# Kernel tuning notes

Hardware: AMD Instinct MI355X
Metric: run time of the kernel (lower is better)

Reference implementation:

```python
import jax, jax.numpy as jnp
import numpy as np

N = 100000   # nodes
E = 1600000  # edges (avg degree 16)
D = 256      # in_channels == dim (forward hard-codes BatchNorm1d(256))
BN_EPS = 1e-5


def _batchnorm(x, gamma, beta):
    # training-mode BatchNorm1d: batch statistics over node dim, biased variance
    mu = jnp.mean(x, axis=0)
    var = jnp.var(x, axis=0)
    return (x - mu) * jax.lax.rsqrt(var + BN_EPS) * gamma + beta


def _gin_conv(x, src, dst, n, W1, b1, gamma, beta, W2, b2):
    # GINConv, eps=0: nn((1+eps)*x + sum_{j in N(i)} x_j)
    agg = jax.ops.segment_sum(x[src], dst, num_segments=n)  # sparse neighbor sum
    h = x + agg
    h = jax.nn.relu(_batchnorm(h @ W1 + b1, gamma, beta))
    return jax.nn.relu(h @ W2 + b2)


def setup_inputs() -> dict:
    key = jax.random.key(0)
    ks = jax.random.split(key, 8)
    x = jax.random.normal(ks[0], (N, D), dtype=jnp.float32)
    edge_index = jax.random.randint(ks[1], (2, E), 0, N, dtype=jnp.int64)
    s = 0.02
    inp = {
        "x": x,
        "edge_index": edge_index,
        # fresh BatchNorm1d(256) in forward (default affine params)
        "g0": jnp.ones((D,), jnp.float32),
        "b0": jnp.zeros((D,), jnp.float32),
        # conv1 MLP: Linear-BN-ReLU-Linear-ReLU
        "W1a": jax.random.normal(ks[2], (D, D), jnp.float32) * s,
        "b1a": jnp.zeros((D,), jnp.float32),
        "g1": jnp.ones((D,), jnp.float32),
        "bt1": jnp.zeros((D,), jnp.float32),
        "W1b": jax.random.normal(ks[3], (D, D), jnp.float32) * s,
        "b1b": jnp.zeros((D,), jnp.float32),
        # conv2 MLP
        "W2a": jax.random.normal(ks[4], (D, D), jnp.float32) * s,
        "b2a": jnp.zeros((D,), jnp.float32),
        "g2": jnp.ones((D,), jnp.float32),
        "bt2": jnp.zeros((D,), jnp.float32),
        "W2b": jax.random.normal(ks[5], (D, D), jnp.float32) * s,
        "b2b": jnp.zeros((D,), jnp.float32),
    }
    return inp


def reference(x, edge_index, g0, b0, W1a, b1a, g1, bt1, W1b, b1b,
              W2a, b2a, g2, bt2, W2b, b2b):
    n = x.shape[0]
    src, dst = edge_index[0], edge_index[1]
    h = _batchnorm(x, g0, b0)                       # fresh BN(256) on input
    h = _gin_conv(h, src, dst, n, W1a, b1a, g1, bt1, W1b, b1b)
    h = jax.nn.relu(h)                              # outer relu (dropout=eval, identity)
    h = _gin_conv(h, src, dst, n, W2a, b2a, g2, bt2, W2b, b2b)
    return jax.nn.relu(h)
```

## Files before the change

### kernel.cpp

```cpp
#include <hip/hip_runtime.h>

#define N_NODES 100000
#define N_EDGES 1600000
#define DIM 256
#define NBINS 196
#define BINCAP 16384

typedef unsigned short bf16u;
typedef __attribute__((ext_vector_type(8))) short bf16x8s;
typedef __attribute__((ext_vector_type(4))) float f32x4;

__device__ __forceinline__ float bf2f(unsigned int u16) {
    union { unsigned int i; float f; } x; x.i = u16 << 16; return x.f;
}
__device__ __forceinline__ float hi2f(unsigned int u) {
    union { unsigned int i; float f; } x; x.i = u & 0xffff0000u; return x.f;
}
__device__ __forceinline__ float lo2f(unsigned int u) {
    union { unsigned int i; float f; } x; x.i = u << 16; return x.f;
}
__device__ __forceinline__ bf16u f2bf(float f) {
    union { float f; unsigned int i; } x; x.f = f;
    unsigned int i = x.i;
    return (bf16u)((i + 0x7fffu + ((i >> 16) & 1u)) >> 16);
}
__device__ __forceinline__ float loadv(const void* p, size_t i, int isf32) {
    return isf32 ? ((const float*)p)[i] : bf2f(((const bf16u*)p)[i]);
}
__device__ __forceinline__ void async_copy16(const void* g, void* l) {
    __builtin_amdgcn_global_load_lds((const __attribute__((address_space(1))) void*)g,
                                     (__attribute__((address_space(3))) void*)l, 16, 0, 0);
}

__global__ void detect_flags(const unsigned* xw, const int* ei, int* flags, int* gBinFill,
                             float* sums) {
    __shared__ int cnt, nz;
    if (threadIdx.x == 0) { cnt = 0; nz = 0; }
    __syncthreads();
    gBinFill[threadIdx.x] = 0;
#pragma unroll
    for (int i = 0; i < 6; ++i) sums[i * 256 + threadIdx.x] = 0.f;
    unsigned u = xw[threadIdx.x];
    float av = fabsf(bf2f(u & 0xffffu));
    if (av > 1e-5f && av < 50.f) atomicAdd(&cnt, 1);
    if (ei[2 * threadIdx.x + 1] != 0) atomicAdd(&nz, 1);
    __syncthreads();
    if (threadIdx.x == 0) {
        flags[0] = (cnt >= 128) ? 0 : 1;
        if (nz == 0) { flags[1] = 2; flags[2] = 2 * N_EDGES; }
        else         { flags[1] = 1; flags[2] = N_EDGES; }
    }
}

__global__ void transpose_w(const void* W0, const void* W1, const void* W2, const void* W3,
                            bf16u* Wt, const int* flags) {
    __shared__ bf16u tile[64][65];
    int isf32 = flags[0];
    const void* W = (blockIdx.y == 0) ? W0 : (blockIdx.y == 1) ? W1 : (blockIdx.y == 2) ? W2 : W3;
    bf16u* out = Wt + (size_t)blockIdx.y * DIM * DIM;
    int t = threadIdx.x;
    int tx = t & 63, ty = t >> 6;
    int k0 = (blockIdx.x >> 2) * 64, n0 = (blockIdx.x & 3) * 64;
#pragma unroll
    for (int i = 0; i < 16; ++i) {
        int r = ty + i * 4;
        tile[tx][r] = f2bf(loadv(W, (size_t)(k0 + r) * DIM + (n0 + tx), isf32));
    }
    __syncthreads();
#pragma unroll
    for (int i = 0; i < 16; ++i) {
        int r = ty + i * 4;
        out[(size_t)(n0 + r) * DIM + (k0 + tx)] = tile[r][tx];
    }
}

__global__ __launch_bounds__(256) void bin_scatter(const int* __restrict__ ei,
                                                   const int* __restrict__ flags,
                                                   uint2* __restrict__ gRec,
                                                   int* __restrict__ gBinFill) {
    __shared__ int cnt[256];
    __shared__ int cur[256];
    __shared__ uint2 rec[4096];
    int t = threadIdx.x;
    cnt[t] = 0; cur[t] = 0;
    __syncthreads();
    int st = flags[1], ofs = flags[2];
    int e0 = blockIdx.x * 4096;
#pragma unroll
    for (int i = 0; i < 16; ++i) {
        int e = e0 + i * 256 + t;
        uint2 r;
        if (e < N_EDGES) {
            r.x = (unsigned)ei[(size_t)ofs + (size_t)e * st];
            r.y = (unsigned)ei[(size_t)e * st];
            atomicAdd(&cnt[r.x >> 9], 1);
        } else {
            r.x = 0xffffffffu; r.y = 0;
        }
        rec[i * 256 + t] = r;
    }
    __syncthreads();
    if (t < NBINS) {
        int c = cnt[t];
        int b = (c > 0) ? atomicAdd(&gBinFill[t], c) : 0;
        cnt[t] = b;
    }
    __syncthreads();
#pragma unroll
    for (int i = 0; i < 16; ++i) {
        uint2 r = rec[i * 256 + t];
        if (r.x != 0xffffffffu) {
            int b = r.x >> 9;
            int li = atomicAdd(&cur[b], 1);
            int pos = cnt[b] + li;
            if (pos < BINCAP) gRec[(size_t)b * BINCAP + pos] = r;
        }
    }
}

__global__ void bin_scan(const int* gBinFill, int* binBase) {
    __shared__ int s[256];
    int t = threadIdx.x;
    s[t] = (t < NBINS) ? gBinFill[t] : 0;
    __syncthreads();
    for (int off = 1; off < 256; off <<= 1) {
        int v = (t >= off) ? s[t - off] : 0;
        __syncthreads();
        s[t] += v;
        __syncthreads();
    }
    binBase[t + 1] = s[t];
    if (t == 0) binBase[0] = 0;
}

__global__ __launch_bounds__(256) void bin_csr(const uint2* __restrict__ gRec,
                                               const int* __restrict__ gBinFill,
                                               const int* __restrict__ binBase,
                                               int* __restrict__ rp, int* __restrict__ col) {
    __shared__ int cntA[512], scanB[512], noff[512], ncur[512];
    int bin = blockIdx.x, t = threadIdx.x;
    int cnt = gBinFill[bin];
    if (cnt > BINCAP) cnt = BINCAP;
    int gbase = binBase[bin], lo = bin << 9;
    cntA[t] = 0; cntA[t + 256] = 0; ncur[t] = 0; ncur[t + 256] = 0;
    __syncthreads();
    const uint2* R = gRec + (size_t)bin * BINCAP;
    for (int j = t; j < cnt; j += 256) atomicAdd(&cntA[(int)R[j].x - lo], 1);
    __syncthreads();
    scanB[t] = cntA[t]; scanB[t + 256] = cntA[t + 256];
    __syncthreads();
    for (int off = 1; off < 512; off <<= 1) {
        int v0 = (t >= off) ? scanB[t - off] : 0;
        int v1 = (t + 256 >= off) ? scanB[t + 256 - off] : 0;
        __syncthreads();
        scanB[t] += v0; scanB[t + 256] += v1;
        __syncthreads();
    }
    noff[t] = scanB[t] - cntA[t];
    noff[t + 256] = scanB[t + 256] - cntA[t + 256];
    __syncthreads();
    int n0 = lo + t, n1 = lo + t + 256;
    if (n0 < N_NODES) rp[n0] = gbase + noff[t];
    if (n1 < N_NODES) rp[n1] = gbase + noff[t + 256];
    if (bin == 0 && t == 0) rp[N_NODES] = N_EDGES;
    for (int j = t; j < cnt; j += 256) {
        uint2 r = R[j];
        int k = (int)r.x - lo;
        int li = atomicAdd(&ncur[k], 1);
        col[gbase + noff[k] + li] = (int)r.y;
    }
}

__global__ void col_stats(const void* X, int nrows, float* sums, const int* flags, int dual) {
    __shared__ float ls[512];
    int isf32 = dual ? flags[0] : 0;
    int t = threadIdx.x;
    ls[t] = 0.f; ls[t + 256] = 0.f;
    __syncthreads();
    int rpb = (nrows + gridDim.x - 1) / gridDim.x;
    int r0 = blockIdx.x * rpb;
    int r1 = r0 + rpb; if (r1 > nrows) r1 = nrows;
    int cg = (t & 31) * 8;
    float s[8], q[8];
#pragma unroll
    for (int j = 0; j < 8; ++j) { s[j] = 0.f; q[j] = 0.f; }
    if (isf32) {
        for (int r = r0 + (t >> 5); r < r1; r += 8) {
            const float* xp = (const float*)X + (size_t)r * DIM + cg;
            f32x4 a = *(const f32x4*)xp, b = *(const f32x4*)(xp + 4);
#pragma unroll
            for (int j = 0; j < 4; ++j) {
                s[j] += a[j]; q[j] += a[j] * a[j];
                s[4 + j] += b[j]; q[4 + j] += b[j] * b[j];
            }
        }
    } else {
        for (int r = r0 + (t >> 5); r < r1; r += 8) {
            size_t base = (size_t)r * DIM + cg;
#pragma unroll
            for (int j = 0; j < 8; ++j) {
                float f = bf2f(((const bf16u*)X)[base + j]);
                s[j] += f; q[j] += f * f;
            }
        }
    }
#pragma unroll
    for (int j = 0; j < 8; ++j) {
        atomicAdd(&ls[cg + j], s[j]);
        atomicAdd(&ls[256 + cg + j], q[j]);
    }
    __syncthreads();
    atomicAdd(&sums[t], ls[t]);
    atomicAdd(&sums[256 + t], ls[256 + t]);
}

__global__ void bn_finalize(const float* sums, const void* gamma, const void* beta,
                            float* sc, float* sh, float inv_n, const int* flags) {
    int isf32 = flags[0];
    int t = threadIdx.x;
    float mu = sums[t] * inv_n;
    float var = sums[256 + t] * inv_n - mu * mu;
    float rs = rsqrtf(var + 1e-5f);
    float g = loadv(gamma, t, isf32), b = loadv(beta, t, isf32);
    sc[t] = rs * g;
    sh[t] = b - mu * rs * g;
}

__global__ void bn_apply(const void* X, const float* sc, const float* sh, bf16u* Y,
                         const int* flags, int dual, int relu) {
    int isf32 = dual ? flags[0] : 0;
    size_t i = (size_t)blockIdx.x * 256 + threadIdx.x;
    int c = ((int)(i & 31)) * 8;
    size_t base = i * 8;
    float v[8];
    if (isf32) {
        f32x4 x0 = *(const f32x4*)((const float*)X + base);
        f32x4 x1 = *(const f32x4*)((const float*)X + base + 4);
#pragma unroll
        for (int j = 0; j < 4; ++j) { v[j] = x0[j]; v[4 + j] = x1[j]; }
    } else {
        uint4 u = *(const uint4*)((const bf16u*)X + base);
        v[0] = lo2f(u.x); v[1] = hi2f(u.x);
        v[2] = lo2f(u.y); v[3] = hi2f(u.y);
        v[4] = lo2f(u.z); v[5] = hi2f(u.z);
        v[6] = lo2f(u.w); v[7] = hi2f(u.w);
    }
    f32x4 s0 = *(const f32x4*)(sc + c), s1 = *(const f32x4*)(sc + c + 4);
    f32x4 h0 = *(const f32x4*)(sh + c), h1 = *(const f32x4*)(sh + c + 4);
    float y[8];
#pragma unroll
    for (int j = 0; j < 4; ++j) {
        y[j]     = v[j]     * s0[j] + h0[j];
        y[4 + j] = v[4 + j] * s1[j] + h1[j];
    }
    if (relu) {
#pragma unroll
        for (int j = 0; j < 8; ++j) y[j] = fmaxf(y[j], 0.f);
    }
    uint4 ov;
    ov.x = (unsigned)f2bf(y[0]) | ((unsigned)f2bf(y[1]) << 16);
    ov.y = (unsigned)f2bf(y[2]) | ((unsigned)f2bf(y[3]) << 16);
    ov.z = (unsigned)f2bf(y[4]) | ((unsigned)f2bf(y[5]) << 16);
    ov.w = (unsigned)f2bf(y[6]) | ((unsigned)f2bf(y[7]) << 16);
    *(uint4*)(Y + base) = ov;
}

__global__ __launch_bounds__(512) void agg_gemm(const bf16u* __restrict__ h,
                                                const int* __restrict__ rp,
                                                const int* __restrict__ col,
                                                const bf16u* __restrict__ Wt,
                                                const void* __restrict__ bias,
                                                bf16u* __restrict__ Cout,
                                                const int* __restrict__ flags,
                                                float* __restrict__ stats) {
    __shared__ __align__(16) bf16u aggA[64 * 256];
    __shared__ __align__(16) bf16u Bs[4 * 256 * 8];
    __shared__ float lsum[512];
    int isf32 = flags[0];
    int t = threadIdx.x;
    int w = t >> 6, lane = t & 63;
    lsum[t] = 0.f;
    int rb = blockIdx.x * 64;

#pragma unroll
    for (int j = 0; j < 2; ++j) {
        int idx = w * 2 + j;
        int chunk = idx & 3, r0 = (idx >> 2) * 64;
        async_copy16(Wt + (size_t)(r0 + lane) * 256 + chunk * 8,
                     &Bs[chunk * 2048 + r0 * 8]);
    }

    {
        int p = lane >> 5, c = lane & 31;
        const uint4* hv = (const uint4*)h;
        for (int i = 0; i < 8; ++i) {
            int lrow = w * 8 + i;
            int node = rb + lrow;
            if (node >= N_NODES) node = N_NODES - 1;
            float acc[8];
            if (p == 0) {
                uint4 u = hv[(size_t)node * 32 + c];
                acc[0] = lo2f(u.x); acc[1] = hi2f(u.x);
                acc[2] = lo2f(u.y); acc[3] = hi2f(u.y);
                acc[4] = lo2f(u.z); acc[5] = hi2f(u.z);
                acc[6] = lo2f(u.w); acc[7] = hi2f(u.w);
            } else {
#pragma unroll
                for (int j = 0; j < 8; ++j) acc[j] = 0.f;
            }
            int e = rp[node], e1 = rp[node + 1];
            for (; e + 8 <= e1; e += 8) {
                int s0 = col[e + p], s1 = col[e + 2 + p], s2 = col[e + 4 + p], s3 = col[e + 6 + p];
                uint4 a = hv[(size_t)s0 * 32 + c];
                uint4 b = hv[(size_t)s1 * 32 + c];
                uint4 d = hv[(size_t)s2 * 32 + c];
                uint4 f = hv[(size_t)s3 * 32 + c];
                acc[0] += lo2f(a.x); acc[1] += hi2f(a.x); acc[2] += lo2f(a.y); acc[3] += hi2f(a.y);
                acc[4] += lo2f(a.z); acc[5] += hi2f(a.z); acc[6] += lo2f(a.w); acc[7] += hi2f(a.w);
                acc[0] += lo2f(b.x); acc[1] += hi2f(b.x); acc[2] += lo2f(b.y); acc[3] += hi2f(b.y);
                acc[4] += lo2f(b.z); acc[5] += hi2f(b.z); acc[6] += lo2f(b.w); acc[7] += hi2f(b.w);
                acc[0] += lo2f(d.x); acc[1] += hi2f(d.x); acc[2] += lo2f(d.y); acc[3] += hi2f(d.y);
                acc[4] += lo2f(d.z); acc[5] += hi2f(d.z); acc[6] += lo2f(d.w); acc[7] += hi2f(d.w);
                acc[0] += lo2f(f.x); acc[1] += hi2f(f.x); acc[2] += lo2f(f.y); acc[3] += hi2f(f.y);
                acc[4] += lo2f(f.z); acc[5] += hi2f(f.z); acc[6] += lo2f(f.w); acc[7] += hi2f(f.w);
            }
            for (; e + 4 <= e1; e += 4) {
                int s0 = col[e + p], s1 = col[e + 2 + p];
                uint4 a = hv[(size_t)s0 * 32 + c];
                uint4 b = hv[(size_t)s1 * 32 + c];
                acc[0] += lo2f(a.x); acc[1] += hi2f(a.x); acc[2] += lo2f(a.y); acc[3] += hi2f(a.y);
                acc[4] += lo2f(a.z); acc[5] += hi2f(a.z); acc[6] += lo2f(a.w); acc[7] += hi2f(a.w);
                acc[0] += lo2f(b.x); acc[1] += hi2f(b.x); acc[2] += lo2f(b.y); acc[3] += hi2f(b.y);
                acc[4] += lo2f(b.z); acc[5] += hi2f(b.z); acc[6] += lo2f(b.w); acc[7] += hi2f(b.w);
            }
            for (; e < e1; e += 2) {
                int idx = e + p;
                if (idx < e1) {
                    uint4 a = hv[(size_t)col[idx] * 32 + c];
                    acc[0] += lo2f(a.x); acc[1] += hi2f(a.x); acc[2] += lo2f(a.y); acc[3] += hi2f(a.y);
                    acc[4] += lo2f(a.z); acc[5] += hi2f(a.z); acc[6] += lo2f(a.w); acc[7] += hi2f(a.w);
                }
            }
#pragma unroll
            for (int j = 0; j < 8; ++j) acc[j] += __shfl_xor(acc[j], 32);
            if (p == 0) {
                uint4 ov;
                ov.x = (unsigned)f2bf(acc[0]) | ((unsigned)f2bf(acc[1]) << 16);
                ov.y = (unsigned)f2bf(acc[2]) | ((unsigned)f2bf(acc[3]) << 16);
                ov.z = (unsigned)f2bf(acc[4]) | ((unsigned)f2bf(acc[5]) << 16);
                ov.w = (unsigned)f2bf(acc[6]) | ((unsigned)f2bf(acc[7]) << 16);
                *(uint4*)&aggA[lrow * 256 + ((c ^ (lrow & 7)) * 8)] = ov;
            }
        }
    }

    int lr = lane & 15, lq = lane >> 4;
    int wm = w >> 2, wn = w & 3;
    f32x4 acc[2][4] = {};
    for (int kk = 0; kk < 8; ++kk) {
        __syncthreads();
        if (kk > 0) {
#pragma unroll
            for (int j = 0; j < 2; ++j) {
                int idx = w * 2 + j;
                int chunk = idx & 3, r0 = (idx >> 2) * 64;
                async_copy16(Wt + (size_t)(r0 + lane) * 256 + kk * 32 + chunk * 8,
                             &Bs[chunk * 2048 + r0 * 8]);
            }
        }
        __syncthreads();
        bf16x8s af[2], bfv[4];
#pragma unroll
        for (int mt = 0; mt < 2; ++mt) {
            int ar = wm * 32 + mt * 16 + lr;
            int kc = kk * 4 + lq;
            af[mt] = *(const bf16x8s*)&aggA[ar * 256 + ((kc ^ (lr & 7)) * 8)];
        }
#pragma unroll
        for (int nt = 0; nt < 4; ++nt) {
            int br = wn * 64 + nt * 16 + lr;
            bfv[nt] = *(const bf16x8s*)&Bs[lq * 2048 + br * 8];
        }
#pragma unroll
        for (int mt = 0; mt < 2; ++mt)
#pragma unroll
            for (int nt = 0; nt < 4; ++nt)
                acc[mt][nt] = __builtin_amdgcn_mfma_f32_16x16x32_bf16(af[mt], bfv[nt], acc[mt][nt], 0, 0, 0);
    }

#pragma unroll
    for (int nt = 0; nt < 4; ++nt) {
        int c = wn * 64 + nt * 16 + lr;
        float bv = loadv(bias, c, isf32);
        float ssum = 0.f, ssq = 0.f;
#pragma unroll
        for (int mt = 0; mt < 2; ++mt) {
            int r0 = rb + wm * 32 + mt * 16 + lq * 4;
#pragma unroll
            for (int j = 0; j < 4; ++j) {
                int r = r0 + j;
                if (r < N_NODES) {
                    float y = acc[mt][nt][j] + bv;
                    Cout[(size_t)r * 256 + c] = f2bf(y);
                    ssum += y; ssq += y * y;
                }
            }
        }
        atomicAdd(&lsum[c], ssum);
        atomicAdd(&lsum[256 + c], ssq);
    }
    __syncthreads();
    if (t < 256) {
        atomicAdd(&stats[t], lsum[t]);
        atomicAdd(&stats[256 + t], lsum[256 + t]);
    }
}

__global__ __launch_bounds__(256) void gemm_bias(const bf16u* __restrict__ A,
                                                 const bf16u* __restrict__ Wt,
                                                 const void* __restrict__ bias,
                                                 void* __restrict__ Cout, int mrows,
                                                 const int* __restrict__ flags,
                                                 int relu, int f32out,
                                                 float* __restrict__ stats,
                                                 const float* __restrict__ bnsc,
                                                 const float* __restrict__ bnsh) {
    __shared__ bf16u As[2][128 * 64];
    __shared__ bf16u Bs[2][128 * 64];
    __shared__ float lsum[256];
    int isf32 = flags[0];
    int t = threadIdx.x;
    int w = t >> 6, lane = t & 63;
    int lr = lane & 15, lq = lane >> 4;
    int wm = w >> 1, wn = w & 1;
    int xcd = blockIdx.x & 7, j0 = blockIdx.x >> 3;
    int wkid = ((xcd < 4) ? xcd * 196 : 784 + (xcd - 4) * 195) + j0;
    int rowBase = (wkid >> 1) * 128, colBase = (wkid & 1) * 128;
    f32x4 acc[4][4] = {};
    lsum[t] = 0.f;
    int srow = t >> 3;
    int g8   = ((t & 7) ^ ((t >> 3) & 7)) * 8;
    int ldsOff = (t >> 3) * 64 + (t & 7) * 8;

    if (bnsc) {
        f32x4 s0v = *(const f32x4*)(bnsc + g8);
        f32x4 s1v = *(const f32x4*)(bnsc + g8 + 4);
        f32x4 h0v = *(const f32x4*)(bnsh + g8);
        f32x4 h1v = *(const f32x4*)(bnsh + g8 + 4);
#pragma unroll
        for (int p = 0; p < 4; ++p) {
            int r = p * 32 + srow;
            int gr = rowBase + r; gr = (gr < mrows) ? gr : (mrows - 1);
            uint4 av = *(const uint4*)(A + (size_t)gr * 256 + g8);
            uint4 ov;
            ov.x = (unsigned)f2bf(fmaxf(lo2f(av.x) * s0v[0] + h0v[0], 0.f)) |
                   ((unsigned)f2bf(fmaxf(hi2f(av.x) * s0v[1] + h0v[1], 0.f)) << 16);
            ov.y = (unsigned)f2bf(fmaxf(lo2f(av.y) * s0v[2] + h0v[2], 0.f)) |
                   ((unsigned)f2bf(fmaxf(hi2f(av.y) * s0v[3] + h0v[3], 0.f)) << 16);
            ov.z = (unsigned)f2bf(fmaxf(lo2f(av.z) * s1v[0] + h1v[0], 0.f)) |
                   ((unsigned)f2bf(fmaxf(hi2f(av.z) * s1v[1] + h1v[1], 0.f)) << 16);
            ov.w = (unsigned)f2bf(fmaxf(lo2f(av.w) * s1v[2] + h1v[2], 0.f)) |
                   ((unsigned)f2bf(fmaxf(hi2f(av.w) * s1v[3] + h1v[3], 0.f)) << 16);
            *(uint4*)&As[0][p * 2048 + ldsOff] = ov;
            async_copy16(Wt + (size_t)(colBase + r) * 256 + g8, &Bs[0][(p * 32 + (w << 3)) * 64]);
        }
    } else {
#pragma unroll
        for (int p = 0; p < 4; ++p) {
            int r = p * 32 + srow;
            int gr = rowBase + r; gr = (gr < mrows) ? gr : (mrows - 1);
            async_copy16(A + (size_t)gr * 256 + g8, &As[0][(p * 32 + (w << 3)) * 64]);
            async_copy16(Wt + (size_t)(colBase + r) * 256 + g8, &Bs[0][(p * 32 + (w << 3)) * 64]);
        }
    }

    for (int kt = 0; kt < 4; ++kt) {
        int b = kt & 1, bn = b ^ 1;
        int kn = (kt + 1) * 64;
        __syncthreads();
        uint4 av[4];
        if (kt < 3) {
            if (bnsc) {
#pragma unroll
                for (int p = 0; p < 4; ++p) {
                    int r = p * 32 + srow;
                    int gr = rowBase + r; gr = (gr < mrows) ? gr : (mrows - 1);
                    av[p] = *(const uint4*)(A + (size_t)gr * 256 + kn + g8);
                }
#pragma unroll
                for (int p = 0; p < 4; ++p) {
                    int r = p * 32 + srow;
                    async_copy16(Wt + (size_t)(colBase + r) * 256 + kn + g8,
                                 &Bs[bn][(p * 32 + (w << 3)) * 64]);
                }
            } else {
#pragma unroll
                for (int p = 0; p < 4; ++p) {
                    int r = p * 32 + srow;
                    int gr = rowBase + r; gr = (gr < mrows) ? gr : (mrows - 1);
                    async_copy16(A + (size_t)gr * 256 + kn + g8,
                                 &As[bn][(p * 32 + (w << 3)) * 64]);
                    async_copy16(Wt + (size_t)(colBase + r) * 256 + kn + g8,
                                 &Bs[bn][(p * 32 + (w << 3)) * 64]);
                }
            }
        }
#pragma unroll
        for (int ks = 0; ks < 2; ++ks) {
            bf16x8s af[4], bfv[4];
#pragma unroll
            for (int mt = 0; mt < 4; ++mt) {
                int ar = wm * 64 + mt * 16 + lr;
                af[mt] = *(const bf16x8s*)&As[b][ar * 64 + (((ks * 4 + lq) ^ (lr & 7)) * 8)];
            }
#pragma unroll
            for (int nt = 0; nt < 4; ++nt) {
                int br = wn * 64 + nt * 16 + lr;
                bfv[nt] = *(const bf16x8s*)&Bs[b][br * 64 + (((ks * 4 + lq) ^ (lr & 7)) * 8)];
            }
#pragma unroll
            for (int mt = 0; mt < 4; ++mt)
#pragma unroll
                for (int nt = 0; nt < 4; ++nt)
                    acc[mt][nt] = __builtin_amdgcn_mfma_f32_16x16x32_bf16(af[mt], bfv[nt], acc[mt][nt], 0, 0, 0);
        }
        if (bnsc && kt < 3) {
            f32x4 s0v = *(const f32x4*)(bnsc + kn + g8);
            f32x4 s1v = *(const f32x4*)(bnsc + kn + g8 + 4);
            f32x4 h0v = *(const f32x4*)(bnsh + kn + g8);
            f32x4 h1v = *(const f32x4*)(bnsh + kn + g8 + 4);
#pragma unroll
            for (int p = 0; p < 4; ++p) {
                uint4 ov;
                ov.x = (unsigned)f2bf(fmaxf(lo2f(av[p].x) * s0v[0] + h0v[0], 0.f)) |
                       ((unsigned)f2bf(fmaxf(hi2f(av[p].x) * s0v[1] + h0v[1], 0.f)) << 16);
                ov.y = (unsigned)f2bf(fmaxf(lo2f(av[p].y) * s0v[2] + h0v[2], 0.f)) |
                       ((unsigned)f2bf(fmaxf(hi2f(av[p].y) * s0v[3] + h0v[3], 0.f)) << 16);
                ov.z = (unsigned)f2bf(fmaxf(lo2f(av[p].z) * s1v[0] + h1v[0], 0.f)) |
                       ((unsigned)f2bf(fmaxf(hi2f(av[p].z) * s1v[1] + h1v[1], 0.f)) << 16);
                ov.w = (unsigned)f2bf(fmaxf(lo2f(av[p].w) * s1v[2] + h1v[2], 0.f)) |
                       ((unsigned)f2bf(fmaxf(hi2f(av[p].w) * s1v[3] + h1v[3], 0.f)) << 16);
                *(uint4*)&As[bn][p * 2048 + ldsOff] = ov;
            }
        }
    }

    int storef32 = f32out && isf32;
#pragma unroll
    for (int nt = 0; nt < 4; ++nt) {
        int cl = wn * 64 + nt * 16 + lr;
        int c = colBase + cl;
        float bv = loadv(bias, c, isf32);
#pragma unroll
        for (int mt = 0; mt < 4; ++mt) {
            int r0 = rowBase + wm * 64 + mt * 16 + lq * 4;
#pragma unroll
            for (int j = 0; j < 4; ++j) {
                int r = r0 + j;
                if (r < mrows) {
                    float y = acc[mt][nt][j] + bv;
                    if (relu) y = fmaxf(y, 0.f);
                    if (storef32) ((float*)Cout)[(size_t)r * 256 + c] = y;
                    else          ((bf16u*)Cout)[(size_t)r * 256 + c] = f2bf(y);
                }
            }
        }
    }
    (void)stats;
}

extern "C" void kernel_launch(void* const* d_in, const int* in_sizes, int n_in,
                              void* d_out, int out_size, void* d_ws, size_t ws_size,
                              hipStream_t stream) {
    const void* x   = d_in[0];
    const int*  ei  = (const int*)d_in[1];
    const void* g0  = d_in[2];
    const void* b0  = d_in[3];
    const void* W1a = d_in[4];
    const void* b1a = d_in[5];
    const void* g1  = d_in[6];
    const void* bt1 = d_in[7];
    const void* W1b = d_in[8];
    const void* b1b = d_in[9];
    const void* W2a = d_in[10];
    const void* b2a = d_in[11];
    const void* g2  = d_in[12];
    const void* bt2 = d_in[13];
    const void* W2b = d_in[14];
    const void* b2b = d_in[15];

    char* ws = (char*)d_ws;
    size_t off = 0;
    auto alloc = [&](size_t bytes) {
        char* p = ws + off;
        off += (bytes + 255) & ~(size_t)255;
        return p;
    };
    const size_t FB = (size_t)N_NODES * DIM * 2;
    bf16u* bufA  = (bf16u*)alloc(FB);
    bf16u* bufB  = (bf16u*)alloc(FB);
    bf16u* Wt    = (bf16u*)alloc((size_t)4 * DIM * DIM * 2);
    int*   colA  = (int*)alloc((size_t)N_EDGES * 4);
    int*   rp    = (int*)alloc((size_t)(N_NODES + 1) * 4);
    int*   gBinFill = (int*)alloc(256 * 4);
    int*   binBase  = (int*)alloc(260 * 4);
    float* sums0 = (float*)alloc(512 * 4);
    float* sums1 = (float*)alloc(512 * 4);
    float* sums2 = (float*)alloc(512 * 4);
    float* sc    = (float*)alloc(256 * 4);
    float* sh    = (float*)alloc(256 * 4);
    int*   flags = (int*)alloc(4 * 4);

    uint2* gRec = (uint2*)bufB;

    bf16u* Wt1a = Wt;
    bf16u* Wt1b = Wt + 65536;
    bf16u* Wt2a = Wt + 2 * 65536;
    bf16u* Wt2b = Wt + 3 * 65536;

    const float inv_n = 1.0f / (float)N_NODES;

    detect_flags<<<1, 256, 0, stream>>>((const unsigned*)x, ei, flags, gBinFill, sums0);
    transpose_w<<<dim3(16, 4), 256, 0, stream>>>(W1a, W1b, W2a, W2b, Wt, flags);

    bin_scatter<<<391, 256, 0, stream>>>(ei, flags, gRec, gBinFill);
    bin_scan<<<1, 256, 0, stream>>>(gBinFill, binBase);
    bin_csr<<<NBINS, 256, 0, stream>>>(gRec, gBinFill, binBase, rp, colA);

    col_stats<<<500, 256, 0, stream>>>(x, N_NODES, sums0, flags, 1);
    bn_finalize<<<1, 256, 0, stream>>>(sums0, g0, b0, sc, sh, inv_n, flags);
    bn_apply<<<12500, 256, 0, stream>>>(x, sc, sh, bufB, flags, 1, 0);

    agg_gemm<<<1563, 512, 0, stream>>>(bufB, rp, colA, Wt1a, b1a, bufA, flags, sums1);
    bn_finalize<<<1, 256, 0, stream>>>(sums1, g1, bt1, sc, sh, inv_n, flags);
    gemm_bias<<<1564, 256, 0, stream>>>(bufA, Wt1b, b1b, bufB, N_NODES, flags, 1, 0, nullptr,
                                        sc, sh);

    agg_gemm<<<1563, 512, 0, stream>>>(bufB, rp, colA, Wt2a, b2a, bufA, flags, sums2);
    bn_finalize<<<1, 256, 0, stream>>>(sums2, g2, bt2, sc, sh, inv_n, flags);
    gemm_bias<<<1564, 256, 0, stream>>>(bufA, Wt2b, b2b, d_out, N_NODES, flags, 1, 1, nullptr,
                                        sc, sh);
}
```

Before: 811.7 us.

## Fold BN finalize into consumer kernels and double-buffer weight tiles in agg_gemm

Removes the three single-block bn_finalize launches. bn_apply and gemm_bias now compute the BatchNorm scale and shift from the column sums into shared memory at the start of each block. agg_gemm gets a double-buffered B tile in LDS so the next k-slice load is issued while the current one is multiplied, which removes one barrier per iteration. The cost is redundant per-block finalize arithmetic and more LDS per block, which may reduce occupancy.

Result: no change. 822.6 us (+1.3%).

```diff
diff --git a/kernel.cpp b/kernel.cpp
--- a/kernel.cpp
+++ b/kernel.cpp
@@ -214,22 +214,22 @@
     atomicAdd(&sums[256 + t], ls[256 + t]);
 }
 
-__global__ void bn_finalize(const float* sums, const void* gamma, const void* beta,
-                            float* sc, float* sh, float inv_n, const int* flags) {
+__global__ void bn_apply(const void* X, const float* __restrict__ sums,
+                         const void* gamma, const void* beta, bf16u* Y,
+                         const int* flags, float inv_n) {
+    __shared__ float sc[256], sh[256];
     int isf32 = flags[0];
     int t = threadIdx.x;
-    float mu = sums[t] * inv_n;
-    float var = sums[256 + t] * inv_n - mu * mu;
-    float rs = rsqrtf(var + 1e-5f);
-    float g = loadv(gamma, t, isf32), b = loadv(beta, t, isf32);
-    sc[t] = rs * g;
-    sh[t] = b - mu * rs * g;
-}
-
-__global__ void bn_apply(const void* X, const float* sc, const float* sh, bf16u* Y,
-                         const int* flags, int dual, int relu) {
-    int isf32 = dual ? flags[0] : 0;
-    size_t i = (size_t)blockIdx.x * 256 + threadIdx.x;
+    {
+        float mu = sums[t] * inv_n;
+        float var = sums[256 + t] * inv_n - mu * mu;
+        float rs = rsqrtf(var + 1e-5f);
+        float g = loadv(gamma, t, isf32), b = loadv(beta, t, isf32);
+        sc[t] = rs * g;
+        sh[t] = b - mu * rs * g;
+    }
+    __syncthreads();
+    size_t i = (size_t)blockIdx.x * 256 + t;
     int c = ((int)(i & 31)) * 8;
     size_t base = i * 8;
     float v[8];
@@ -252,10 +252,6 @@
     for (int j = 0; j < 4; ++j) {
         y[j]     = v[j]     * s0[j] + h0[j];
         y[4 + j] = v[4 + j] * s1[j] + h1[j];
-    }
-    if (relu) {
-#pragma unroll
-        for (int j = 0; j < 8; ++j) y[j] = fmaxf(y[j], 0.f);
     }
     uint4 ov;
     ov.x = (unsigned)f2bf(y[0]) | ((unsigned)f2bf(y[1]) << 16);
@@ -274,7 +270,7 @@
                                                 const int* __restrict__ flags,
                                                 float* __restrict__ stats) {
     __shared__ __align__(16) bf16u aggA[64 * 256];
-    __shared__ __align__(16) bf16u Bs[4 * 256 * 8];
+    __shared__ __align__(16) bf16u Bs[2][4 * 256 * 8];
     __shared__ float lsum[512];
     int isf32 = flags[0];
     int t = threadIdx.x;
@@ -282,13 +278,16 @@
     lsum[t] = 0.f;
     int rb = blockIdx.x * 64;
 
-#pragma unroll
-    for (int j = 0; j < 2; ++j) {
-        int idx = w * 2 + j;
-        int chunk = idx & 3, r0 = (idx >> 2) * 64;
-        async_copy16(Wt + (size_t)(r0 + lane) * 256 + chunk * 8,
-                     &Bs[chunk * 2048 + r0 * 8]);
-    }
+    auto stageB = [&](int s, int bb) {
+#pragma unroll
+        for (int j = 0; j < 2; ++j) {
+            int idx = w * 2 + j;
+            int chunk = idx & 3, r0 = (idx >> 2) * 64;
+            async_copy16(Wt + (size_t)(r0 + lane) * 256 + s * 32 + chunk * 8,
+                         &Bs[bb][chunk * 2048 + r0 * 8]);
+        }
+    };
+    stageB(0, 0);
 
     {
         int p = lane >> 5, c = lane & 31;
@@ -358,17 +357,9 @@
     int wm = w >> 2, wn = w & 3;
     f32x4 acc[2][4] = {};
     for (int kk = 0; kk < 8; ++kk) {
+        int cb = kk & 1;
         __syncthreads();
-        if (kk > 0) {
-#pragma unroll
-            for (int j = 0; j < 2; ++j) {
-                int idx = w * 2 + j;
-                int chunk = idx & 3, r0 = (idx >> 2) * 64;
-                async_copy16(Wt + (size_t)(r0 + lane) * 256 + kk * 32 + chunk * 8,
-                             &Bs[chunk * 2048 + r0 * 8]);
-            }
-        }
-        __syncthreads();
+        if (kk < 7) stageB(kk + 1, cb ^ 1);
         bf16x8s af[2], bfv[4];
 #pragma unroll
         for (int mt = 0; mt < 2; ++mt) {
@@ -379,7 +370,7 @@
 #pragma unroll
         for (int nt = 0; nt < 4; ++nt) {
             int br = wn * 64 + nt * 16 + lr;
-            bfv[nt] = *(const bf16x8s*)&Bs[lq * 2048 + br * 8];
+            bfv[nt] = *(const bf16x8s*)&Bs[cb][lq * 2048 + br * 8];
         }
 #pragma unroll
         for (int mt = 0; mt < 2; ++mt)
@@ -422,27 +413,36 @@
                                                  void* __restrict__ Cout, int mrows,
                                                  const int* __restrict__ flags,
                                                  int relu, int f32out,
-                                                 float* __restrict__ stats,
-                                                 const float* __restrict__ bnsc,
-                                                 const float* __restrict__ bnsh) {
+                                                 const float* __restrict__ sums,
+                                                 const void* __restrict__ gamma,
+                                                 const void* __restrict__ beta,
+                                                 float inv_n) {
     __shared__ bf16u As[2][128 * 64];
-    __shared__ bf16u Bs[2][128 * 64];
-    __shared__ float lsum[256];
+    __shared__ bf16u BsS[2][128 * 64];
+    __shared__ float bnsc[256], bnsh[256];
     int isf32 = flags[0];
     int t = threadIdx.x;
     int w = t >> 6, lane = t & 63;
     int lr = lane & 15, lq = lane >> 4;
     int wm = w >> 1, wn = w & 1;
+    {
+        float mu = sums[t] * inv_n;
+        float var = sums[256 + t] * inv_n - mu * mu;
+        float rs = rsqrtf(var + 1e-5f);
+        float g = loadv(gamma, t, isf32), b = loadv(beta, t, isf32);
+        bnsc[t] = rs * g;
+        bnsh[t] = b - mu * rs * g;
+    }
     int xcd = blockIdx.x & 7, j0 = blockIdx.x >> 3;
     int wkid = ((xcd < 4) ? xcd * 196 : 784 + (xcd - 4) * 195) + j0;
     int rowBase = (wkid >> 1) * 128, colBase = (wkid & 1) * 128;
     f32x4 acc[4][4] = {};
-    lsum[t] = 0.f;
     int srow = t >> 3;
     int g8   = ((t & 7) ^ ((t >> 3) & 7)) * 8;
     int ldsOff = (t >> 3) * 64 + (t & 7) * 8;
-
-    if (bnsc) {
+    __syncthreads();
+
+    {
         f32x4 s0v = *(const f32x4*)(bnsc + g8);
         f32x4 s1v = *(const f32x4*)(bnsc + g8 + 4);
         f32x4 h0v = *(const f32x4*)(bnsh + g8);
@@ -462,15 +462,7 @@
             ov.w = (unsigned)f2bf(fmaxf(lo2f(av.w) * s1v[2] + h1v[2], 0.f)) |
                    ((unsigned)f2bf(fmaxf(hi2f(av.w) * s1v[3] + h1v[3], 0.f)) << 16);
             *(uint4*)&As[0][p * 2048 + ldsOff] = ov;
-            async_copy16(Wt + (size_t)(colBase + r) * 256 + g8, &Bs[0][(p * 32 + (w << 3)) * 64]);
-        }
-    } else {
-#pragma unroll
-        for (int p = 0; p < 4; ++p) {
-            int r = p * 32 + srow;
-            int gr = rowBase + r; gr = (gr < mrows) ? gr : (mrows - 1);
-            async_copy16(A + (size_t)gr * 256 + g8, &As[0][(p * 32 + (w << 3)) * 64]);
-            async_copy16(Wt + (size_t)(colBase + r) * 256 + g8, &Bs[0][(p * 32 + (w << 3)) * 64]);
+            async_copy16(Wt + (size_t)(colBase + r) * 256 + g8, &BsS[0][(p * 32 + (w << 3)) * 64]);
         }
     }
 
@@ -480,29 +472,17 @@
         __syncthreads();
         uint4 av[4];
         if (kt < 3) {
-            if (bnsc) {
-#pragma unroll
-                for (int p = 0; p < 4; ++p) {
-                    int r = p * 32 + srow;
-                    int gr = rowBase + r; gr = (gr < mrows) ? gr : (mrows - 1);
-                    av[p] = *(const uint4*)(A + (size_t)gr * 256 + kn + g8);
-                }
-#pragma unroll
-                for (int p = 0; p < 4; ++p) {
-                    int r = p * 32 + srow;
-                    async_copy16(Wt + (size_t)(colBase + r) * 256 + kn + g8,
-                                 &Bs[bn][(p * 32 + (w << 3)) * 64]);
-                }
-            } else {
-#pragma unroll
-                for (int p = 0; p < 4; ++p) {
-                    int r = p * 32 + srow;
-                    int gr = rowBase + r; gr = (gr < mrows) ? gr : (mrows - 1);
-                    async_copy16(A + (size_t)gr * 256 + kn + g8,
-                                 &As[bn][(p * 32 + (w << 3)) * 64]);
-                    async_copy16(Wt + (size_t)(colBase + r) * 256 + kn + g8,
-                                 &Bs[bn][(p * 32 + (w << 3)) * 64]);
-                }
+#pragma unroll
+            for (int p = 0; p < 4; ++p) {
+                int r = p * 32 + srow;
+                int gr = rowBase + r; gr = (gr < mrows) ? gr : (mrows - 1);
+                av[p] = *(const uint4*)(A + (size_t)gr * 256 + kn + g8);
+            }
+#pragma unroll
+            for (int p = 0; p < 4; ++p) {
+                int r = p * 32 + srow;
+                async_copy16(Wt + (size_t)(colBase + r) * 256 + kn + g8,
+                             &BsS[bn][(p * 32 + (w << 3)) * 64]);
             }
         }
 #pragma unroll
@@ -516,7 +496,7 @@
 #pragma unroll
             for (int nt = 0; nt < 4; ++nt) {
                 int br = wn * 64 + nt * 16 + lr;
-                bfv[nt] = *(const bf16x8s*)&Bs[b][br * 64 + (((ks * 4 + lq) ^ (lr & 7)) * 8)];
+                bfv[nt] = *(const bf16x8s*)&BsS[b][br * 64 + (((ks * 4 + lq) ^ (lr & 7)) * 8)];
             }
 #pragma unroll
             for (int mt = 0; mt < 4; ++mt)
@@ -524,7 +504,7 @@
                 for (int nt = 0; nt < 4; ++nt)
                     acc[mt][nt] = __builtin_amdgcn_mfma_f32_16x16x32_bf16(af[mt], bfv[nt], acc[mt][nt], 0, 0, 0);
         }
-        if (bnsc && kt < 3) {
+        if (kt < 3) {
             f32x4 s0v = *(const f32x4*)(bnsc + kn + g8);
             f32x4 s1v = *(const f32x4*)(bnsc + kn + g8 + 4);
             f32x4 h0v = *(const f32x4*)(bnsh + kn + g8);
@@ -566,7 +546,6 @@
             }
         }
     }
-    (void)stats;
 }
 
 extern "C" void kernel_launch(void* const* d_in, const int* in_sizes, int n_in,
@@ -607,8 +586,6 @@
     float* sums0 = (float*)alloc(512 * 4);
     float* sums1 = (float*)alloc(512 * 4);
     float* sums2 = (float*)alloc(512 * 4);
-    float* sc    = (float*)alloc(256 * 4);
-    float* sh    = (float*)alloc(256 * 4);
     int*   flags = (int*)alloc(4 * 4);
 
     uint2* gRec = (uint2*)bufB;
@@ -628,16 +605,13 @@
     bin_csr<<<NBINS, 256, 0, stream>>>(gRec, gBinFill, binBase, rp, colA);
 
     col_stats<<<500, 256, 0, stream>>>(x, N_NODES, sums0, flags, 1);
-    bn_finalize<<<1, 256, 0, stream>>>(sums0, g0, b0, sc, sh, inv_n, flags);
-    bn_apply<<<12500, 256, 0, stream>>>(x, sc, sh, bufB, flags, 1, 0);
+    bn_apply<<<12500, 256, 0, stream>>>(x, sums0, g0, b0, bufB, flags, inv_n);
 
     agg_gemm<<<1563, 512, 0, stream>>>(bufB, rp, colA, Wt1a, b1a, bufA, flags, sums1);
-    bn_finalize<<<1, 256, 0, stream>>>(sums1, g1, bt1, sc, sh, inv_n, flags);
-    gemm_bias<<<1564, 256, 0, stream>>>(bufA, Wt1b, b1b, bufB, N_NODES, flags, 1, 0, nullptr,
-                                        sc, sh);
+    gemm_bias<<<1564, 256, 0, stream>>>(bufA, Wt1b, b1b, bufB, N_NODES, flags, 1, 0,
+                                        sums1, g1, bt1, inv_n);
 
     agg_gemm<<<1563, 512, 0, stream>>>(bufB, rp, colA, Wt2a, b2a, bufA, flags, sums2);
-    bn_finalize<<<1, 256, 0, stream>>>(sums2, g2, bt2, sc, sh, inv_n, flags);
-    gemm_bias<<<1564, 256, 0, stream>>>(bufA, Wt2b, b2b, d_out, N_NODES, flags, 1, 1, nullptr,
-                                        sc, sh);
-}
+    gemm_bias<<<1564, 256, 0, stream>>>(bufA, Wt2b, b2b, d_out, N_NODES, flags, 1, 1,
+                                        sums2, g2, bt2, inv_n);
+}
```
